# Kernel optimization log

Hardware: AMD Instinct MI355X
Metric: run time of the kernel (lower is better)

The kernel has to match this reference:

```python
import jax, jax.numpy as jnp
import numpy as np
from jax import lax

N, C, H, W = 6, 64, 128, 128
BN_EPS = 1e-5


def setup_inputs() -> dict:
    key = jax.random.key(0)
    ks = jax.random.split(key, 16)
    def p(i, shape, scale=0.05):
        return jax.random.normal(ks[i], shape, jnp.float32) * scale
    return {
        "raw_feat": jax.random.normal(ks[0], (N, C, H, W), jnp.float32),
        # PixelWeightedFusionSoftmax params (1x1 convs stored as [out,in] matrices)
        "pw_w1": p(1, (4, C)), "pw_b1": p(2, (4,)),
        "bn_gamma": 1.0 + p(3, (4,)), "bn_beta": p(4, (4,)),
        "bn_mean": jnp.zeros((4,), jnp.float32), "bn_var": jnp.ones((4,), jnp.float32),
        "pw_w2": p(5, (1, 4)), "pw_b2": p(6, (1,)),
        # ConvMod params: a = dwconv11x11(gelu(conv1x1_{2C->C}(q))); out = proj(a * v(v) * att_map)
        "cm_a1_w": p(7, (C, 2 * C)), "cm_a1_b": p(8, (C,)),
        "cm_dw_w": p(9, (C, 1, 11, 11)), "cm_dw_b": p(10, (C,)),
        "cm_v_w": p(11, (C, C)), "cm_v_b": p(12, (C,)),
        "cm_proj_w": p(13, (C, C)), "cm_proj_b": p(14, (C,)),
    }


def _conf_maps(x, pw_w1, pw_b1, bn_gamma, bn_beta, bn_mean, bn_var, pw_w2, pw_b2):
    # x: [N,C,H,W] -> per-agent confidence maps [N,1,H,W], min-max normalized per agent
    h = jnp.einsum('nchw,oc->nohw', x, pw_w1) + pw_b1[:, None, None]
    scale = (bn_gamma / jnp.sqrt(bn_var + BN_EPS))[:, None, None]
    h = (h - bn_mean[:, None, None]) * scale + bn_beta[:, None, None]  # BN eval mode
    h = jax.nn.relu(h)
    h = jax.nn.relu(jnp.einsum('nchw,oc->nohw', h, pw_w2) + pw_b2[:, None, None])
    mn = h.min(axis=(1, 2, 3), keepdims=True)
    mx = h.max(axis=(1, 2, 3), keepdims=True)
    return (h - mn) / (mx - mn)


def reference(raw_feat, pw_w1, pw_b1, bn_gamma, bn_beta, bn_mean, bn_var, pw_w2, pw_b2,
              cm_a1_w, cm_a1_b, cm_dw_w, cm_dw_b, cm_v_w, cm_v_b, cm_proj_w, cm_proj_b):
    conf = _conf_maps(raw_feat, pw_w1, pw_b1, bn_gamma, bn_beta, bn_mean, bn_var, pw_w2, pw_b2)  # [N,1,H,W]
    # att_map[i,k] = (1 - conf_i) * conf_k
    att_map = (1.0 - conf)[:, None] * conf[None, :]  # [N,N,1,H,W]
    # q[i,k] = concat(raw[i], raw[k]) along channels -> [N,N,2C,H,W]
    q = jnp.concatenate([jnp.broadcast_to(raw_feat[:, None], (N, N, C, H, W)),
                         jnp.broadcast_to(raw_feat[None, :], (N, N, C, H, W))], axis=2)
    a = jax.nn.gelu(jnp.einsum('ikchw,oc->ikohw', q, cm_a1_w) + cm_a1_b[:, None, None],
                    approximate=False)
    a = lax.conv_general_dilated(a.reshape(N * N, C, H, W), cm_dw_w,
                                 window_strides=(1, 1), padding='SAME',
                                 feature_group_count=C,
                                 dimension_numbers=('NCHW', 'OIHW', 'NCHW'))
    a = a.reshape(N, N, C, H, W) + cm_dw_b[:, None, None]
    vproj = jnp.einsum('nchw,oc->nohw', raw_feat, cm_v_w) + cm_v_b[:, None, None]  # [N,C,H,W]
    x = a * vproj[None] * att_map  # [N,N,C,H,W]
    out = jnp.einsum('ikchw,oc->ikohw', x, cm_proj_w) + cm_proj_b[:, None, None]
    updated = raw_feat + out.sum(axis=1)  # ego i accumulates over all senders k
    return updated.reshape(N * C, H, W)   # matches torch.cat(local_com_mat_update, dim=0)
```

## Files before the change

kernel.cpp:

```cpp
#include <hip/hip_runtime.h>
#include <hip/hip_fp16.h>
#include <math.h>

#define NAG 6
#define CC  64
#define HH  128
#define WW  128
#define HWT 16384
#define HWP 8192
#define BN_EPS 1e-5f
#define WFRAG_PJ_OFF (24 * 64 * 8)
#define WFRAG_W1_OFF (32 * 64 * 8)

typedef unsigned int u32;
typedef __fp16 f16x2v __attribute__((ext_vector_type(2)));
typedef __fp16 f16x8  __attribute__((ext_vector_type(8)));
typedef float  f32x4  __attribute__((ext_vector_type(4)));

__device__ __forceinline__ u32 gelu_pk(u32 xu) {
    __half2 x = __builtin_bit_cast(__half2, xu);
    __half2 s = __hmul2(x, x);
    __half2 m = __hfma2(s, __float2half2_rn(-0.10294535f),
                        __float2half2_rn(-2.30226045f));
    __half2 e = h2exp2(__hmul2(x, m));
    __half2 r = h2rcp(__hadd2(e, __float2half2_rn(1.0f)));
    return __builtin_bit_cast(u32, __hmul2(x, r));
}

__device__ __forceinline__ float dot8(f16x8 a, f16x8 b, float acc) {
    uint4 au = __builtin_bit_cast(uint4, a);
    uint4 bu = __builtin_bit_cast(uint4, b);
    acc = __builtin_amdgcn_fdot2(__builtin_bit_cast(f16x2v, au.x),
                                 __builtin_bit_cast(f16x2v, bu.x), acc, false);
    acc = __builtin_amdgcn_fdot2(__builtin_bit_cast(f16x2v, au.y),
                                 __builtin_bit_cast(f16x2v, bu.y), acc, false);
    acc = __builtin_amdgcn_fdot2(__builtin_bit_cast(f16x2v, au.z),
                                 __builtin_bit_cast(f16x2v, bu.z), acc, false);
    acc = __builtin_amdgcn_fdot2(__builtin_bit_cast(f16x2v, au.w),
                                 __builtin_bit_cast(f16x2v, bu.w), acc, false);
    return acc;
}

__global__ __launch_bounds__(256) void k_setup(
    const float* __restrict__ a1w, const float* __restrict__ vw,
    const float* __restrict__ pjw, const float* __restrict__ w1,
    __fp16* __restrict__ wfrag, u32* __restrict__ mm)
{
    int t = blockIdx.x * 256 + threadIdx.x;
    if (t < NAG) mm[t] = 0x7F800000u;
    else if (t < 2 * NAG) mm[t] = 0u;
    if (t < 32) {
        int kf = t >> 4, kg = (t >> 2) & 3, o = t & 3;
        const float* src = w1 + o * CC + kf * 32 + kg * 8;
        __fp16* dst = wfrag + WFRAG_W1_OFF + t * 8;
        #pragma unroll
        for (int j = 0; j < 8; ++j) dst[j] = (__fp16)src[j];
    }
    if (t >= 32 * 64) return;
    int lane = t & 63;
    int slot = t >> 6;
    bool pj = slot >= 24;
    int s = pj ? slot - 24 : slot;
    int ot = s >> 1, kf = s & 1;
    int o  = (pj ? ot : (ot & 3)) * 16 + (lane & 15);
    int ch = kf * 32 + (lane >> 4) * 8;
    const float* src;
    if (pj)          src = pjw + o * CC + ch;
    else if (ot < 4) src = a1w + o * 2 * CC + ch;
    else if (ot < 8) src = a1w + o * 2 * CC + CC + ch;
    else             src = vw  + o * CC + ch;
    __fp16* dst = wfrag + ((size_t)slot * 64 + lane) * 8;
    #pragma unroll
    for (int j = 0; j < 8; ++j) dst[j] = (__fp16)src[j];
}

__global__ __launch_bounds__(256) void k_front(
    const float* __restrict__ raw, const __fp16* __restrict__ wfrag,
    const float* __restrict__ vb,
    const float* __restrict__ b1, const float* __restrict__ gamma,
    const float* __restrict__ beta, const float* __restrict__ mean,
    const float* __restrict__ var, const float* __restrict__ w2,
    const float* __restrict__ b2,
    float* __restrict__ conf, u32* __restrict__ mm,
    u32* __restrict__ Ph, u32* __restrict__ Qh, u32* __restrict__ Wh)
{
    const int n   = blockIdx.y;
    const int px0 = blockIdx.x * 128;
    const int t = threadIdx.x, lane = t & 63, wv = t >> 6;
    const int lm = lane & 15, kg = lane >> 4;
    const int pxw = px0 + wv * 32;
    const int pxl = pxw + lm;
    const int pxs = pxw + kg * 4;

    const float* rawn = raw + (size_t)n * CC * HWT;

    f16x8 afr[2][2];
    #pragma unroll
    for (int mt = 0; mt < 2; ++mt) {
        #pragma unroll
        for (int kf = 0; kf < 2; ++kf) {
            const float* base = rawn + (size_t)(kf * 32 + kg * 8) * HWT + pxl + mt * 16;
            f16x8 a;
            #pragma unroll
            for (int p = 0; p < 4; ++p) {
                f16x2v h = __builtin_amdgcn_cvt_pkrtz(base[(2 * p) * HWT],
                                                      base[(2 * p + 1) * HWT]);
                a[2 * p] = h.x; a[2 * p + 1] = h.y;
            }
            afr[mt][kf] = a;
        }
    }

    float h2v[2];
    {
        f16x8 w1v[2][4];
        #pragma unroll
        for (int kf = 0; kf < 2; ++kf)
            #pragma unroll
            for (int o = 0; o < 4; ++o)
                w1v[kf][o] = *(const f16x8*)(wfrag + WFRAG_W1_OFF +
                                             ((kf * 4 + kg) * 4 + o) * 8);
        #pragma unroll
        for (int mt = 0; mt < 2; ++mt) {
            float h1[4];
            #pragma unroll
            for (int o = 0; o < 4; ++o) {
                float a = dot8(w1v[0][o], afr[mt][0], 0.f);
                a = dot8(w1v[1][o], afr[mt][1], a);
                a += __shfl_xor(a, 16, 64);
                a += __shfl_xor(a, 32, 64);
                h1[o] = a;
            }
            float h2 = b2[0];
            #pragma unroll
            for (int o = 0; o < 4; ++o) {
                float sc = gamma[o] * rsqrtf(var[o] + BN_EPS);
                float hb = (h1[o] + b1[o] - mean[o]) * sc + beta[o];
                hb = fmaxf(hb, 0.f);
                h2 = fmaf(w2[o], hb, h2);
            }
            h2v[mt] = fmaxf(h2, 0.f);
        }
        if (kg == 0) {
            conf[n * HWT + pxl]      = h2v[0];
            conf[n * HWT + pxl + 16] = h2v[1];
        }
        float mn = fminf(h2v[0], h2v[1]), mx = fmaxf(h2v[0], h2v[1]);
        #pragma unroll
        for (int off = 32; off > 0; off >>= 1) {
            mn = fminf(mn, __shfl_xor(mn, off, 64));
            mx = fmaxf(mx, __shfl_xor(mx, off, 64));
        }
        __shared__ float smn[4], smx[4];
        if (lane == 0) { smn[wv] = mn; smx[wv] = mx; }
        __syncthreads();
        if (t == 0) {
            mn = fminf(fminf(smn[0], smn[1]), fminf(smn[2], smn[3]));
            mx = fmaxf(fmaxf(smx[0], smx[1]), fmaxf(smx[2], smx[3]));
            atomicMin(&mm[n], __float_as_uint(mn));
            atomicMax(&mm[n + NAG], __float_as_uint(mx));
        }
    }

    #pragma unroll
    for (int ot = 0; ot < 12; ++ot) {
        f16x8 b0 = *(const f16x8*)(wfrag + ((size_t)(ot * 2 + 0) * 64 + lane) * 8);
        f16x8 b1f = *(const f16x8*)(wfrag + ((size_t)(ot * 2 + 1) * 64 + lane) * 8);
        const int o = (ot & 3) * 16 + lm;
        #pragma unroll
        for (int mt = 0; mt < 2; ++mt) {
            f32x4 acc = (f32x4){0.f, 0.f, 0.f, 0.f};
            acc = __builtin_amdgcn_mfma_f32_16x16x32_f16(afr[mt][0], b0, acc, 0, 0, 0);
            acc = __builtin_amdgcn_mfma_f32_16x16x32_f16(afr[mt][1], b1f, acc, 0, 0, 0);
            const int pxb = pxs + mt * 16;
            f32x4 r;
            u32* plane;
            if (ot < 8) {
                r = acc;
                plane = (ot < 4 ? Ph : Qh) + (size_t)(n * CC + o) * HWP + (pxb >> 1);
            } else {
                r = acc + vb[o];
                plane = Wh + (size_t)(n * CC + o) * HWP + (pxb >> 1);
            }
            f16x2v h0 = __builtin_amdgcn_cvt_pkrtz(r[0], r[1]);
            f16x2v h1 = __builtin_amdgcn_cvt_pkrtz(r[2], r[3]);
            *(uint2*)plane = make_uint2(__builtin_bit_cast(u32, h0),
                                        __builtin_bit_cast(u32, h1));
        }
    }
}

#define GPITCH 88
#define GROWS  74
#define GDW    (GROWS * GPITCH / 2)
#define NU2    13

__global__ __launch_bounds__(256, 3) void k_main(
    const u32* __restrict__ Ph, const u32* __restrict__ Qh,
    const u32* __restrict__ Wh, const float* __restrict__ conf,
    const u32* __restrict__ mm,
    const float* __restrict__ a1b, const float* __restrict__ dww,
    const float* __restrict__ dwb, u32* __restrict__ Sh)
{
    const int tile = blockIdx.x;
    const int c    = blockIdx.y;
    const int i    = blockIdx.z;
    const int y0 = (tile >> 1) * 64;
    const int x0 = (tile & 1) * 64;
    const int t    = threadIdx.x;
    const int lane = t & 63;
    const int ty   = t >> 6;
    const int lm   = lane & 15;
    const int kg   = lane >> 4;
    const int kg8  = kg * 8;

    __shared__ __align__(16) u32 GT32[2 * GDW];

    const float bdw = dwb[c];
    const float ba1 = a1b[c];

    const float* wc = dww + c * 121;
    f16x8 afrag[11];
    #pragma unroll
    for (int dy = 0; dy < 11; ++dy) {
        f16x8 a;
        #pragma unroll
        for (int j = 0; j < 8; ++j) {
            int d = kg8 + j - lm - 3;
            int dcl = min(max(d, 0), 10);
            float wv = wc[dy * 11 + dcl];
            a[j] = (__fp16)((d == dcl) ? wv : 0.f);
        }
        afrag[dy] = a;
    }

    f16x2v bias2; bias2.x = (__fp16)ba1; bias2.y = (__fp16)ba1;

    int offs[NU2];
    u32 preg[NU2];
    const u32* Pc = Ph + (size_t)(i * CC + c) * HWP;
    #pragma unroll
    for (int u = 0; u < NU2; ++u) {
        int d = t + u * 256;
        int row = d / (GPITCH / 2);
        int cp  = d - row * (GPITCH / 2);
        int gy = y0 + row - 5;
        int gx = x0 + 2 * cp - 8;
        bool inb = (d < GDW) && (gy >= 0) && (gy < HH) && (gx >= 0) && (gx < WW);
        offs[u] = inb ? (gy * (WW / 2) + (gx >> 1)) : -1;
        u32 p = 0u;
        if (inb) {
            f16x2v ph = __builtin_bit_cast(f16x2v, Pc[offs[u]]) + bias2;
            p = __builtin_bit_cast(u32, ph);
        }
        preg[u] = p;
    }

    const int oy  = y0 + ty * 16 + lm;
    const int obx = x0 + kg * 4;
    const int obase = oy * WW + obx;
    const int rowb = (ty * 16 + lm) * GPITCH + kg8;

    f32x4 sacc[4];
    #pragma unroll
    for (int tx = 0; tx < 4; ++tx) sacc[tx] = (f32x4){0.f, 0.f, 0.f, 0.f};

    u32 qreg[NU2];
    {
        const u32* Qc = Qh + (size_t)(0 * CC + c) * HWP;
        #pragma unroll
        for (int u = 0; u < NU2; ++u)
            qreg[u] = (offs[u] >= 0) ? Qc[offs[u]] : 0u;
    }
    #pragma unroll
    for (int u = 0; u < NU2; ++u) {
        int d = t + u * 256;
        if (u < NU2 - 1 || d < GDW) {
            f16x2v s = __builtin_bit_cast(f16x2v, preg[u]) +
                       __builtin_bit_cast(f16x2v, qreg[u]);
            GT32[d] = gelu_pk(__builtin_bit_cast(u32, s));
        }
    }
    {
        const u32* Qc = Qh + (size_t)(1 * CC + c) * HWP;
        #pragma unroll
        for (int u = 0; u < NU2; ++u)
            qreg[u] = (offs[u] >= 0) ? Qc[offs[u]] : 0u;
    }
    __syncthreads();

    #pragma unroll 1
    for (int k = 0; k < NAG; ++k) {
        const __fp16* GTh = (const __fp16*)(GT32 + (k & 1) * GDW);
        u32* GW = GT32 + ((k + 1) & 1) * GDW;
        const bool dog = (k + 1 < NAG);
        const bool doq = (k + 2 < NAG);
        const u32* Qc2 = Qh + (size_t)((doq ? k + 2 : 0) * CC + c) * HWP;
        const u32* Wc  = Wh + (size_t)(k * CC + c) * HWP + (obase >> 1);
        const float* cfk = conf + (size_t)k * HWT + obase;

        const float mnk = __uint_as_float(mm[k]);
        const float mxk = __uint_as_float(mm[k + NAG]);
        const float invk = 1.f / (mxk - mnk);

        #pragma unroll
        for (int tx = 0; tx < 4; ++tx) {
            uint2 wvt = *(const uint2*)(Wc + 8 * tx);
            f32x4 cf4 = *(const f32x4*)(cfk + 16 * tx);
            f32x4 acc = (f32x4){0.f, 0.f, 0.f, 0.f};
            __builtin_amdgcn_s_setprio(1);
            #pragma unroll
            for (int dy = 0; dy < 11; ++dy) {
                f16x8 b = *(const f16x8*)(GTh + rowb + dy * GPITCH + 16 * tx);
                acc = __builtin_amdgcn_mfma_f32_16x16x32_f16(afrag[dy], b, acc, 0, 0, 0);
            }
            __builtin_amdgcn_s_setprio(0);
            f16x2v w0 = __builtin_bit_cast(f16x2v, wvt.x);
            f16x2v w1 = __builtin_bit_cast(f16x2v, wvt.y);
            f32x4 wf = (f32x4){(float)w0.x, (float)w0.y, (float)w1.x, (float)w1.y};
            wf *= (cf4 - mnk) * invk;
            sacc[tx] += (acc + bdw) * wf;

            if (dog) {
                const int u0 = (tx == 3) ? 9 : tx * 3;
                const int u1 = (tx == 3) ? NU2 : tx * 3 + 3;
                #pragma unroll
                for (int u = u0; u < u1; ++u) {
                    int d = t + u * 256;
                    if (u < NU2 - 1 || d < GDW) {
                        f16x2v s = __builtin_bit_cast(f16x2v, preg[u]) +
                                   __builtin_bit_cast(f16x2v, qreg[u]);
                        GW[d] = gelu_pk(__builtin_bit_cast(u32, s));
                        if (doq) qreg[u] = (offs[u] >= 0) ? Qc2[offs[u]] : 0u;
                    }
                }
            }
        }

        if (dog) __syncthreads();
    }

    const float mn = __uint_as_float(mm[i]);
    const float mx = __uint_as_float(mm[i + NAG]);
    const float inv = 1.f / (mx - mn);
    const float* cfi = conf + i * HWT + obase;
    u32* Sc = Sh + (size_t)(i * CC + c) * HWP + (obase >> 1);
    #pragma unroll
    for (int tx = 0; tx < 4; ++tx) {
        f32x4 cv = *(const f32x4*)(cfi + 16 * tx);
        f32x4 r = sacc[tx] * (1.f - (cv - mn) * inv);
        f16x2v h0 = __builtin_amdgcn_cvt_pkrtz(r[0], r[1]);
        f16x2v h1 = __builtin_amdgcn_cvt_pkrtz(r[2], r[3]);
        *(uint2*)(Sc + 8 * tx) = make_uint2(__builtin_bit_cast(u32, h0),
                                            __builtin_bit_cast(u32, h1));
    }
}

__global__ __launch_bounds__(256) void k_out(
    const u32* __restrict__ Sh, const float* __restrict__ raw,
    const __fp16* __restrict__ wfrag, const float* __restrict__ pb,
    float* __restrict__ out)
{
    const int n   = blockIdx.y;
    const int px0 = blockIdx.x * 128;
    const int t = threadIdx.x, lane = t & 63, wv = t >> 6;
    const int lm = lane & 15, kg = lane >> 4;
    const int pxw = px0 + wv * 32;
    const int pxl = pxw + lm;
    const int pxs = pxw + kg * 4;

    const u32* Sn = Sh + (size_t)n * CC * HWP;
    const u32 sh = (pxl & 1) * 16;

    f16x8 afr[2][2];
    #pragma unroll
    for (int mt = 0; mt < 2; ++mt) {
        #pragma unroll
        for (int kf = 0; kf < 2; ++kf) {
            const u32* base = Sn + (size_t)(kf * 32 + kg * 8) * HWP + ((pxl + mt * 16) >> 1);
            f16x8 a;
            #pragma unroll
            for (int j = 0; j < 8; ++j) {
                unsigned short v = (unsigned short)(base[(size_t)j * HWP] >> sh);
                a[j] = __builtin_bit_cast(__fp16, v);
            }
            afr[mt][kf] = a;
        }
    }

    #pragma unroll
    for (int ot = 0; ot < 4; ++ot) {
        f16x8 b0 = *(const f16x8*)(wfrag + WFRAG_PJ_OFF +
                                   ((size_t)(ot * 2 + 0) * 64 + lane) * 8);
        f16x8 b1 = *(const f16x8*)(wfrag + WFRAG_PJ_OFF +
                                   ((size_t)(ot * 2 + 1) * 64 + lane) * 8);
        const int o = ot * 16 + lm;
        const float bias = (float)NAG * pb[o];
        #pragma unroll
        for (int mt = 0; mt < 2; ++mt) {
            f32x4 acc = (f32x4){0.f, 0.f, 0.f, 0.f};
            acc = __builtin_amdgcn_mfma_f32_16x16x32_f16(afr[mt][0], b0, acc, 0, 0, 0);
            acc = __builtin_amdgcn_mfma_f32_16x16x32_f16(afr[mt][1], b1, acc, 0, 0, 0);
            const int pxb = pxs + mt * 16;
            f32x4 r = *(const f32x4*)(raw + (size_t)(n * CC + o) * HWT + pxb);
            f32x4 ov = r + acc + bias;
            *(f32x4*)(out + (size_t)(n * CC + o) * HWT + pxb) = ov;
        }
    }
}

extern "C" void kernel_launch(void* const* d_in, const int* in_sizes, int n_in,
                              void* d_out, int out_size, void* d_ws, size_t ws_size,
                              hipStream_t stream)
{
    (void)in_sizes; (void)n_in; (void)out_size; (void)ws_size;

    const float* raw   = (const float*)d_in[0];
    const float* pw_w1 = (const float*)d_in[1];
    const float* pw_b1 = (const float*)d_in[2];
    const float* bng   = (const float*)d_in[3];
    const float* bnb   = (const float*)d_in[4];
    const float* bnm   = (const float*)d_in[5];
    const float* bnv   = (const float*)d_in[6];
    const float* pw_w2 = (const float*)d_in[7];
    const float* pw_b2 = (const float*)d_in[8];
    const float* a1w   = (const float*)d_in[9];
    const float* a1b   = (const float*)d_in[10];
    const float* dww   = (const float*)d_in[11];
    const float* dwb   = (const float*)d_in[12];
    const float* vw    = (const float*)d_in[13];
    const float* vb    = (const float*)d_in[14];
    const float* pjw   = (const float*)d_in[15];
    const float* pjb   = (const float*)d_in[16];

    float* ws   = (float*)d_ws;
    float* conf = ws;
    u32*   mm   = (u32*)(ws + NAG * HWT);
    u32*   Ph   = (u32*)(ws + NAG * HWT + 16);
    u32*   Qh   = Ph + (size_t)NAG * CC * HWP;
    u32*   Wh   = Qh + (size_t)NAG * CC * HWP;
    u32*   Sh   = Wh + (size_t)NAG * CC * HWP;
    __fp16* wfrag = (__fp16*)(Sh + (size_t)NAG * CC * HWP);
    float* out  = (float*)d_out;

    k_setup<<<dim3(8), dim3(256), 0, stream>>>(a1w, vw, pjw, pw_w1, wfrag, mm);
    k_front<<<dim3(HWT / 128, NAG), dim3(256), 0, stream>>>(
        raw, wfrag, vb, pw_b1, bng, bnb, bnm, bnv, pw_w2, pw_b2,
        conf, mm, Ph, Qh, Wh);
    k_main<<<dim3(4, CC, NAG), dim3(256), 0, stream>>>(Ph, Qh, Wh, conf, mm, a1b, dww, dwb, Sh);
    k_out<<<dim3(HWT / 128, NAG), dim3(256), 0, stream>>>(Sh, raw, wfrag, pjb, out);
}
```

Measured before the change: 111.8 us.

## Precompute v*conf plane in front kernel and split MFMA accumulator chain

```diff
diff --git a/kernel.cpp b/kernel.cpp
--- a/kernel.cpp
+++ b/kernel.cpp
@@ -82,7 +82,8 @@
     const float* __restrict__ var, const float* __restrict__ w2,
     const float* __restrict__ b2,
     float* __restrict__ conf, u32* __restrict__ mm,
-    u32* __restrict__ Ph, u32* __restrict__ Qh, u32* __restrict__ Wh)
+    u32* __restrict__ Ph, u32* __restrict__ Qh,
+    u32* __restrict__ Wh, u32* __restrict__ WCh)
 {
     const int n   = blockIdx.y;
     const int px0 = blockIdx.x * 128;
@@ -162,9 +163,16 @@
         }
     }
 
+    f32x4 cf[2];
+    #pragma unroll
+    for (int mt = 0; mt < 2; ++mt)
+        #pragma unroll
+        for (int j = 0; j < 4; ++j)
+            cf[mt][j] = __shfl(h2v[mt], (lane & 0x30) | (kg * 4 + j), 64);
+
     #pragma unroll
     for (int ot = 0; ot < 12; ++ot) {
-        f16x8 b0 = *(const f16x8*)(wfrag + ((size_t)(ot * 2 + 0) * 64 + lane) * 8);
+        f16x8 b0  = *(const f16x8*)(wfrag + ((size_t)(ot * 2 + 0) * 64 + lane) * 8);
         f16x8 b1f = *(const f16x8*)(wfrag + ((size_t)(ot * 2 + 1) * 64 + lane) * 8);
         const int o = (ot & 3) * 16 + lm;
         #pragma unroll
@@ -173,19 +181,26 @@
             acc = __builtin_amdgcn_mfma_f32_16x16x32_f16(afr[mt][0], b0, acc, 0, 0, 0);
             acc = __builtin_amdgcn_mfma_f32_16x16x32_f16(afr[mt][1], b1f, acc, 0, 0, 0);
             const int pxb = pxs + mt * 16;
-            f32x4 r;
-            u32* plane;
             if (ot < 8) {
-                r = acc;
-                plane = (ot < 4 ? Ph : Qh) + (size_t)(n * CC + o) * HWP + (pxb >> 1);
+                u32* plane = (ot < 4 ? Ph : Qh) + (size_t)(n * CC + o) * HWP + (pxb >> 1);
+                f16x2v h0 = __builtin_amdgcn_cvt_pkrtz(acc[0], acc[1]);
+                f16x2v h1 = __builtin_amdgcn_cvt_pkrtz(acc[2], acc[3]);
+                *(uint2*)plane = make_uint2(__builtin_bit_cast(u32, h0),
+                                            __builtin_bit_cast(u32, h1));
             } else {
-                r = acc + vb[o];
-                plane = Wh + (size_t)(n * CC + o) * HWP + (pxb >> 1);
-            }
-            f16x2v h0 = __builtin_amdgcn_cvt_pkrtz(r[0], r[1]);
-            f16x2v h1 = __builtin_amdgcn_cvt_pkrtz(r[2], r[3]);
-            *(uint2*)plane = make_uint2(__builtin_bit_cast(u32, h0),
-                                        __builtin_bit_cast(u32, h1));
+                f32x4 r = acc + vb[o];
+                f32x4 rc = r * cf[mt];
+                u32* pw  = Wh  + (size_t)(n * CC + o) * HWP + (pxb >> 1);
+                u32* pwc = WCh + (size_t)(n * CC + o) * HWP + (pxb >> 1);
+                f16x2v h0 = __builtin_amdgcn_cvt_pkrtz(r[0], r[1]);
+                f16x2v h1 = __builtin_amdgcn_cvt_pkrtz(r[2], r[3]);
+                *(uint2*)pw = make_uint2(__builtin_bit_cast(u32, h0),
+                                         __builtin_bit_cast(u32, h1));
+                f16x2v c0 = __builtin_amdgcn_cvt_pkrtz(rc[0], rc[1]);
+                f16x2v c1 = __builtin_amdgcn_cvt_pkrtz(rc[2], rc[3]);
+                *(uint2*)pwc = make_uint2(__builtin_bit_cast(u32, c0),
+                                          __builtin_bit_cast(u32, c1));
+            }
         }
     }
 }
@@ -197,8 +212,8 @@
 
 __global__ __launch_bounds__(256, 3) void k_main(
     const u32* __restrict__ Ph, const u32* __restrict__ Qh,
-    const u32* __restrict__ Wh, const float* __restrict__ conf,
-    const u32* __restrict__ mm,
+    const u32* __restrict__ Wh, const u32* __restrict__ WCh,
+    const float* __restrict__ conf, const u32* __restrict__ mm,
     const float* __restrict__ a1b, const float* __restrict__ dww,
     const float* __restrict__ dwb, u32* __restrict__ Sh)
 {
@@ -296,30 +311,38 @@
         const bool dog = (k + 1 < NAG);
         const bool doq = (k + 2 < NAG);
         const u32* Qc2 = Qh + (size_t)((doq ? k + 2 : 0) * CC + c) * HWP;
-        const u32* Wc  = Wh + (size_t)(k * CC + c) * HWP + (obase >> 1);
-        const float* cfk = conf + (size_t)k * HWT + obase;
-
-        const float mnk = __uint_as_float(mm[k]);
-        const float mxk = __uint_as_float(mm[k + NAG]);
-        const float invk = 1.f / (mxk - mnk);
+        const u32* Wc  = Wh  + (size_t)(k * CC + c) * HWP + (obase >> 1);
+        const u32* WCc = WCh + (size_t)(k * CC + c) * HWP + (obase >> 1);
+
+        const float mnk  = __uint_as_float(mm[k]);
+        const float invk = 1.f / (__uint_as_float(mm[k + NAG]) - mnk);
+        const float mnivk = mnk * invk;
 
         #pragma unroll
         for (int tx = 0; tx < 4; ++tx) {
-            uint2 wvt = *(const uint2*)(Wc + 8 * tx);
-            f32x4 cf4 = *(const f32x4*)(cfk + 16 * tx);
-            f32x4 acc = (f32x4){0.f, 0.f, 0.f, 0.f};
+            uint2 wvt  = *(const uint2*)(Wc + 8 * tx);
+            uint2 wvtc = *(const uint2*)(WCc + 8 * tx);
+            f32x4 acc0 = (f32x4){0.f, 0.f, 0.f, 0.f};
+            f32x4 acc1 = (f32x4){0.f, 0.f, 0.f, 0.f};
             __builtin_amdgcn_s_setprio(1);
             #pragma unroll
             for (int dy = 0; dy < 11; ++dy) {
                 f16x8 b = *(const f16x8*)(GTh + rowb + dy * GPITCH + 16 * tx);
-                acc = __builtin_amdgcn_mfma_f32_16x16x32_f16(afrag[dy], b, acc, 0, 0, 0);
+                if (dy & 1)
+                    acc1 = __builtin_amdgcn_mfma_f32_16x16x32_f16(afrag[dy], b, acc1, 0, 0, 0);
+                else
+                    acc0 = __builtin_amdgcn_mfma_f32_16x16x32_f16(afrag[dy], b, acc0, 0, 0, 0);
             }
             __builtin_amdgcn_s_setprio(0);
-            f16x2v w0 = __builtin_bit_cast(f16x2v, wvt.x);
-            f16x2v w1 = __builtin_bit_cast(f16x2v, wvt.y);
-            f32x4 wf = (f32x4){(float)w0.x, (float)w0.y, (float)w1.x, (float)w1.y};
-            wf *= (cf4 - mnk) * invk;
-            sacc[tx] += (acc + bdw) * wf;
+            f32x4 acc = acc0 + acc1;
+            f16x2v w0  = __builtin_bit_cast(f16x2v, wvt.x);
+            f16x2v w1  = __builtin_bit_cast(f16x2v, wvt.y);
+            f16x2v wc0 = __builtin_bit_cast(f16x2v, wvtc.x);
+            f16x2v wc1 = __builtin_bit_cast(f16x2v, wvtc.y);
+            f32x4 wf  = (f32x4){(float)w0.x, (float)w0.y, (float)w1.x, (float)w1.y};
+            f32x4 wfc = (f32x4){(float)wc0.x, (float)wc0.y, (float)wc1.x, (float)wc1.y};
+            f32x4 weff = wfc * invk - wf * mnivk;
+            sacc[tx] += (acc + bdw) * weff;
 
             if (dog) {
                 const int u0 = (tx == 3) ? 9 : tx * 3;
@@ -439,14 +462,16 @@
     u32*   Ph   = (u32*)(ws + NAG * HWT + 16);
     u32*   Qh   = Ph + (size_t)NAG * CC * HWP;
     u32*   Wh   = Qh + (size_t)NAG * CC * HWP;
-    u32*   Sh   = Wh + (size_t)NAG * CC * HWP;
+    u32*   WCh  = Wh + (size_t)NAG * CC * HWP;
+    u32*   Sh   = WCh + (size_t)NAG * CC * HWP;
     __fp16* wfrag = (__fp16*)(Sh + (size_t)NAG * CC * HWP);
     float* out  = (float*)d_out;
 
     k_setup<<<dim3(8), dim3(256), 0, stream>>>(a1w, vw, pjw, pw_w1, wfrag, mm);
     k_front<<<dim3(HWT / 128, NAG), dim3(256), 0, stream>>>(
         raw, wfrag, vb, pw_b1, bng, bnb, bnm, bnv, pw_w2, pw_b2,
-        conf, mm, Ph, Qh, Wh);
-    k_main<<<dim3(4, CC, NAG), dim3(256), 0, stream>>>(Ph, Qh, Wh, conf, mm, a1b, dww, dwb, Sh);
+        conf, mm, Ph, Qh, Wh, WCh);
+    k_main<<<dim3(4, CC, NAG), dim3(256), 0, stream>>>(Ph, Qh, Wh, WCh, conf, mm,
+                                                       a1b, dww, dwb, Sh);
     k_out<<<dim3(HWT / 128, NAG), dim3(256), 0, stream>>>(Sh, raw, wfrag, pjb, out);
 }
```

Result: slower. 127.0 us (+13.6%).
